# Kernel optimization log

Hardware: AMD Instinct MI355X
Metric: run time of the kernel (lower is better)

The kernel has to match this reference:

```python
import jax, jax.numpy as jnp
import numpy as np

N_NODES = 100000


def sage_conv(x, src, dst, W_l, b_l, W_r):
    # PyG SAGEConv (aggr='mean'): out = lin_l(mean_j x_j) + lin_r(x_i)
    msg = x[src]  # [E, d] gather of source-node features
    agg = jax.ops.segment_sum(msg, dst, num_segments=N_NODES)  # [N, d]
    deg = jax.ops.segment_sum(jnp.ones((src.shape[0],), x.dtype), dst,
                              num_segments=N_NODES)
    mean = agg / jnp.clip(deg, 1.0, None)[:, None]
    return mean @ W_l.T + b_l + x @ W_r.T


def setup_inputs() -> dict:
    key = jax.random.key(0)
    ks = jax.random.split(key, 12)
    d_in, d_h, d_out, n_edges = 64, 64, 2, 1200000
    s = 1.0 / np.sqrt(d_h)
    inp = {
        "x": jax.random.normal(ks[0], (N_NODES, d_in), dtype=jnp.float32),
        "edge_index": jax.random.randint(ks[1], (2, n_edges), 0, N_NODES,
                                         dtype=jnp.int64),
        "W_l1": jax.random.uniform(ks[2], (d_h, d_in), jnp.float32, -s, s),
        "b_l1": jax.random.uniform(ks[3], (d_h,), jnp.float32, -s, s),
        "W_r1": jax.random.uniform(ks[4], (d_h, d_in), jnp.float32, -s, s),
        "W_l2": jax.random.uniform(ks[5], (d_h, d_h), jnp.float32, -s, s),
        "b_l2": jax.random.uniform(ks[6], (d_h,), jnp.float32, -s, s),
        "W_r2": jax.random.uniform(ks[7], (d_h, d_h), jnp.float32, -s, s),
        "W_c": jax.random.uniform(ks[8], (d_out, d_h), jnp.float32, -s, s),
        "b_c": jax.random.uniform(ks[9], (d_out,), jnp.float32, -s, s),
    }
    return inp


def reference(x, edge_index, W_l1, b_l1, W_r1, W_l2, b_l2, W_r2, W_c, b_c):
    src, dst = edge_index[0], edge_index[1]
    # layer 1 + relu (dropout is identity in eval mode)
    h = jax.nn.relu(sage_conv(x, src, dst, W_l1, b_l1, W_r1))
    # layer 2 (no relu per forward())
    h = sage_conv(h, src, dst, W_l2, b_l2, W_r2)
    # classifier
    return h @ W_c.T + b_c
```

## Files before the change

### kernel.cpp

```cpp
#include <hip/hip_runtime.h>

#define N_NODES 100000
#define D 64
#define NTILES 3125
#define NBUCK 391
#define NBLK_A 512
#define GCNT_N (NBUCK * NBLK_A)
#define NCHUNK ((GCNT_N + 255) / 256)
#define NTILE_T (N_NODES / 32)
#define TROW 72

typedef __attribute__((ext_vector_type(8))) short short8;
typedef __attribute__((ext_vector_type(16))) float f32x16;
union Pack8 { uint4 u; short8 s; };

__device__ __forceinline__ unsigned f2bf(float f) {
  unsigned u = __float_as_uint(f);
  return (u + 0x7fffu + ((u >> 16) & 1u)) >> 16;
}
#define BF_LO(u) __uint_as_float(((unsigned)(u)) << 16)
#define BF_HI(u) __uint_as_float(((unsigned)(u)) & 0xffff0000u)


__global__ __launch_bounds__(256) void passA_count(const int* __restrict__ dst,
                                                   int* __restrict__ gcnt,
                                                   int nE, int ec) {
  __shared__ int cnt[NBUCK];
  int t = threadIdx.x, blk = blockIdx.x;
  for (int i = t; i < NBUCK; i += 256) cnt[i] = 0;
  __syncthreads();
  int e0 = blk * ec, e1 = min(e0 + ec, nE);
  for (int e = e0 + t; e < e1; e += 256) atomicAdd(&cnt[dst[e] >> 8], 1);
  __syncthreads();
  for (int b = t; b < NBUCK; b += 256) gcnt[b * NBLK_A + blk] = cnt[b];
}

__global__ void gscan_p1(const int* __restrict__ g, int* __restrict__ csum) {
  int t = threadIdx.x, b = blockIdx.x;
  int i = b * 256 + t;
  int v = (i < GCNT_N) ? g[i] : 0;
  for (int off = 32; off; off >>= 1) v += __shfl_down(v, off);
  __shared__ int ws4[4];
  if ((t & 63) == 0) ws4[t >> 6] = v;
  __syncthreads();
  if (t == 0) csum[b] = ws4[0] + ws4[1] + ws4[2] + ws4[3];
}

__global__ void gscan_p2(int* __restrict__ csum, int nB) {
  __shared__ int s[1024];
  int t = threadIdx.x;
  int orig = (t < nB) ? csum[t] : 0;
  s[t] = orig;
  __syncthreads();
  for (int off = 1; off < 1024; off <<= 1) {
    int v = (t >= off) ? s[t - off] : 0;
    __syncthreads();
    s[t] += v;
    __syncthreads();
  }
  if (t < nB) csum[t] = s[t] - orig;
}

__global__ void gscan_p3(int* __restrict__ g, const int* __restrict__ csum) {
  __shared__ int s[256];
  int t = threadIdx.x, b = blockIdx.x;
  int i = b * 256 + t;
  int d = (i < GCNT_N) ? g[i] : 0;
  s[t] = d;
  __syncthreads();
  for (int off = 1; off < 256; off <<= 1) {
    int v = (t >= off) ? s[t - off] : 0;
    __syncthreads();
    s[t] += v;
    __syncthreads();
  }
  if (i < GCNT_N) g[i] = s[t] - d + csum[b];
}

__global__ __launch_bounds__(256) void passC_place(const int* __restrict__ src,
                                                   const int* __restrict__ dst,
                                                   const int* __restrict__ S,
                                                   uint2* __restrict__ pairs,
                                                   int nE, int ec) {
  __shared__ int cur[NBUCK];
  int t = threadIdx.x, blk = blockIdx.x;
  for (int b = t; b < NBUCK; b += 256) cur[b] = S[b * NBLK_A + blk];
  __syncthreads();
  int e0 = blk * ec, e1 = min(e0 + ec, nE);
  for (int e = e0 + t; e < e1; e += 256) {
    int d = dst[e];
    int p = atomicAdd(&cur[d >> 8], 1);
    pairs[p] = make_uint2((unsigned)d, (unsigned)src[e]);
  }
}

__global__ __launch_bounds__(256) void passD_csr(const uint2* __restrict__ pairs,
                                                 const int* __restrict__ S,
                                                 int* __restrict__ rowstart,
                                                 int* __restrict__ degI,
                                                 uint2* __restrict__ srt,
                                                 int nE) {
  __shared__ int lh[256];
  __shared__ int sc[256];
  __shared__ int cur[256];
  int t = threadIdx.x, b = blockIdx.x;
  int base = S[b * NBLK_A];
  int end = (b == NBUCK - 1) ? nE : S[(b + 1) * NBLK_A];
  lh[t] = 0;
  __syncthreads();
  for (int p = base + t; p < end; p += 256) atomicAdd(&lh[pairs[p].x & 255], 1);
  __syncthreads();
  int d = lh[t];
  sc[t] = d;
  __syncthreads();
  for (int off = 1; off < 256; off <<= 1) {
    int v = (t >= off) ? sc[t - off] : 0;
    __syncthreads();
    sc[t] += v;
    __syncthreads();
  }
  int ex = sc[t] - d;
  int node = b * 256 + t;
  if (node < N_NODES) {
    rowstart[node] = base + ex;
    degI[node] = d;
  }
  cur[t] = base + ex;
  __syncthreads();
  for (int p = base + t; p < end; p += 256) {
    uint2 e = pairs[p];
    int slot = atomicAdd(&cur[e.x & 255], 1);
    srt[slot] = e;
  }
}

__global__ __launch_bounds__(256) void prep_kernel(
    const float* __restrict__ Wc, const float* __restrict__ Wl2,
    const float* __restrict__ Wr2, const float* __restrict__ bl2,
    const float* __restrict__ bc, const float* __restrict__ Wl1,
    const float* __restrict__ Wr1, float* __restrict__ A2,
    float* __restrict__ B2, float* __restrict__ bfv,
    unsigned short* __restrict__ wcat) {
  int t = threadIdx.x;
  for (int i = t; i < 8192; i += 256)
    wcat[i] = (unsigned short)f2bf((i < 4096) ? Wl1[i] : Wr1[i - 4096]);
  if (t < 128) {
    int c = t >> 6, k = t & 63;
    float sa = 0.f, sb = 0.f;
    for (int j = 0; j < 64; ++j) {
      float w = Wc[c * 64 + j];
      sa = fmaf(w, Wl2[j * 64 + k], sa);
      sb = fmaf(w, Wr2[j * 64 + k], sb);
    }
    A2[c * 64 + k] = sa;
    B2[c * 64 + k] = sb;
  }
  if (t < 2) {
    float s = bc[t];
    for (int j = 0; j < 64; ++j) s = fmaf(Wc[t * 64 + j], bl2[j], s);
    bfv[t] = s;
  }
}

__global__ __launch_bounds__(256) void transform_mfma(
    const float* __restrict__ x, const unsigned short* __restrict__ wcat,
    const float* __restrict__ bl, unsigned short* __restrict__ t1,
    unsigned short* __restrict__ r1b) {
  int tid = threadIdx.x, lane = tid & 63;
  int l31 = lane & 31, hi = lane >> 5;

  short8 af[4][4];
#pragma unroll
  for (int jt = 0; jt < 4; ++jt)
#pragma unroll
    for (int kk = 0; kk < 4; ++kk)
      af[jt][kk] = *(const short8*)(wcat + (jt * 32 + l31) * 64 + kk * 16 + 8 * hi);

  const f32x16 Z = {0.f, 0.f, 0.f, 0.f, 0.f, 0.f, 0.f, 0.f,
                    0.f, 0.f, 0.f, 0.f, 0.f, 0.f, 0.f, 0.f};
  const float4* x4 = (const float4*)x;

  int gw = (blockIdx.x * 256 + tid) >> 6;
  int nW = (gridDim.x * 256) >> 6;

  for (int tile = gw; tile < NTILE_T; tile += nW) {
    int node = tile * 32 + l31;
    f32x16 acc[4] = {Z, Z, Z, Z};
#pragma unroll
    for (int kk = 0; kk < 4; ++kk) {
      float4 fa = x4[(size_t)node * 16 + kk * 4 + 2 * hi];
      float4 fb = x4[(size_t)node * 16 + kk * 4 + 2 * hi + 1];
      Pack8 pk;
      pk.u.x = f2bf(fa.x) | (f2bf(fa.y) << 16);
      pk.u.y = f2bf(fa.z) | (f2bf(fa.w) << 16);
      pk.u.z = f2bf(fb.x) | (f2bf(fb.y) << 16);
      pk.u.w = f2bf(fb.z) | (f2bf(fb.w) << 16);
      acc[0] = __builtin_amdgcn_mfma_f32_32x32x16_bf16(af[0][kk], pk.s, acc[0], 0, 0, 0);
      acc[1] = __builtin_amdgcn_mfma_f32_32x32x16_bf16(af[1][kk], pk.s, acc[1], 0, 0, 0);
      acc[2] = __builtin_amdgcn_mfma_f32_32x32x16_bf16(af[2][kk], pk.s, acc[2], 0, 0, 0);
      acc[3] = __builtin_amdgcn_mfma_f32_32x32x16_bf16(af[3][kk], pk.s, acc[3], 0, 0, 0);
    }
#pragma unroll
    for (int jt = 0; jt < 2; ++jt)
#pragma unroll
      for (int rg = 0; rg < 4; ++rg) {
        int j0 = jt * 32 + 8 * rg + 4 * hi;
        uint2 p;
        p.x = f2bf(acc[jt][4 * rg + 0]) | (f2bf(acc[jt][4 * rg + 1]) << 16);
        p.y = f2bf(acc[jt][4 * rg + 2]) | (f2bf(acc[jt][4 * rg + 3]) << 16);
        *(uint2*)(t1 + (size_t)node * 64 + j0) = p;
      }
#pragma unroll
    for (int jt = 2; jt < 4; ++jt)
#pragma unroll
      for (int rg = 0; rg < 4; ++rg) {
        int j0 = (jt - 2) * 32 + 8 * rg + 4 * hi;
        float4 bv = ((const float4*)bl)[j0 >> 2];
        uint2 p;
        p.x = f2bf(acc[jt][4 * rg + 0] + bv.x) |
              (f2bf(acc[jt][4 * rg + 1] + bv.y) << 16);
        p.y = f2bf(acc[jt][4 * rg + 2] + bv.z) |
              (f2bf(acc[jt][4 * rg + 3] + bv.w) << 16);
        *(uint2*)(r1b + (size_t)node * 64 + j0) = p;
      }
  }
}

__global__ __launch_bounds__(256) void tile_g1(
    const uint2* __restrict__ srt, const int* __restrict__ rowstart,
    const unsigned short* __restrict__ t1,
    const unsigned short* __restrict__ r1b, const float* __restrict__ A2,
    const float* __restrict__ B2, float2* __restrict__ g2,
    float2* __restrict__ s2, int nE) {
  __shared__ float pAB[4][64];
  __shared__ unsigned short stg[4][2][16 * TROW];
  __shared__ int ideg[4][64];
  int t = threadIdx.x, lane = t & 63, w = t >> 6;
  pAB[t >> 6][t & 63] = (t < 128) ? A2[t] : B2[t - 128];
  __syncthreads();

  int tile = blockIdx.x;
  int base = rowstart[tile * 32];
  int end = (tile == NTILES - 1) ? nE : rowstart[(tile + 1) * 32];
  int l31 = lane & 31, hi = lane >> 5;
  int o = lane >> 3, j8 = lane & 7;
  unsigned short* stA = &stg[w][0][0];
  unsigned short* stB = &stg[w][1][0];

  int ngAll = (end > base) ? ((end - base + 15) >> 4) : 0;
  int gper = (ngAll + 3) >> 2;
  int wbase = base + min(w * gper, ngAll) * 16;
  int wend = min(base + min((w + 1) * gper, ngAll) * 16, end);

  const f32x16 Z = {0.f, 0.f, 0.f, 0.f, 0.f, 0.f, 0.f, 0.f,
                    0.f, 0.f, 0.f, 0.f, 0.f, 0.f, 0.f, 0.f};
  f32x16 acc0 = Z, acc1 = Z;
  int degc = 0;
  int ng = (wend > wbase) ? ((wend - wbase + 15) >> 4) : 0;

  uint2 prA = make_uint2(0u, 0u), prB = make_uint2(0u, 0u);
  int cntA = 0, cntB = 0;
  uint4 vA0 = make_uint4(0, 0, 0, 0), vA1 = vA0, vB0 = vA0, vB1 = vA0;
  if (ng > 0) {
    prA = srt[min(wbase + (lane & 15), nE - 1)];
    cntA = min(wend - wbase, 16);
    int s0 = __shfl((int)prA.y, o), s1 = __shfl((int)prA.y, 8 + o);
    vA0 = *(const uint4*)(t1 + (size_t)((o < cntA) ? s0 : 0) * 64 + j8 * 8);
    vA1 = *(const uint4*)(t1 + (size_t)((8 + o < cntA) ? s1 : 0) * 64 + j8 * 8);
  }
  if (ng > 1) {
    int nb = wbase + 16;
    prB = srt[min(nb + (lane & 15), nE - 1)];
    cntB = min(wend - nb, 16);
    int s0 = __shfl((int)prB.y, o), s1 = __shfl((int)prB.y, 8 + o);
    vB0 = *(const uint4*)(t1 + (size_t)((o < cntB) ? s0 : 0) * 64 + j8 * 8);
    vB1 = *(const uint4*)(t1 + (size_t)((8 + o < cntB) ? s1 : 0) * 64 + j8 * 8);
  }

  for (int gg = 0; gg < ng; gg += 2) {
    bool hasB = (gg + 1 < ng);
    *(uint4*)(stA + o * TROW + j8 * 8) = vA0;
    *(uint4*)(stA + (8 + o) * TROW + j8 * 8) = vA1;
    if (hasB) {
      *(uint4*)(stB + o * TROW + j8 * 8) = vB0;
      *(uint4*)(stB + (8 + o) * TROW + j8 * 8) = vB1;
    }
    unsigned amA[8], amB[8];
#pragma unroll
    for (int m = 0; m < 8; ++m) {
      int e = 8 * hi + m;
      int dv = __shfl((int)prA.x, e);
      bool ok = (e < cntA) && ((dv & 31) == l31);
      amA[m] = ok ? 0x3F80u : 0u;
      degc += (amA[m] >> 7) & 1;
    }
    if (hasB) {
#pragma unroll
      for (int m = 0; m < 8; ++m) {
        int e = 8 * hi + m;
        int dv = __shfl((int)prB.x, e);
        bool ok = (e < cntB) && ((dv & 31) == l31);
        amB[m] = ok ? 0x3F80u : 0u;
        degc += (amB[m] >> 7) & 1;
      }
    }
    if (gg + 2 < ng) {
      int nb = wbase + (gg + 2) * 16;
      prA = srt[min(nb + (lane & 15), nE - 1)];
      cntA = min(wend - nb, 16);
      int s0 = __shfl((int)prA.y, o), s1 = __shfl((int)prA.y, 8 + o);
      vA0 = *(const uint4*)(t1 + (size_t)((o < cntA) ? s0 : 0) * 64 + j8 * 8);
      vA1 = *(const uint4*)(t1 + (size_t)((8 + o < cntA) ? s1 : 0) * 64 + j8 * 8);
    }
    if (gg + 3 < ng) {
      int nb = wbase + (gg + 3) * 16;
      prB = srt[min(nb + (lane & 15), nE - 1)];
      cntB = min(wend - nb, 16);
      int s0 = __shfl((int)prB.y, o), s1 = __shfl((int)prB.y, 8 + o);
      vB0 = *(const uint4*)(t1 + (size_t)((o < cntB) ? s0 : 0) * 64 + j8 * 8);
      vB1 = *(const uint4*)(t1 + (size_t)((8 + o < cntB) ? s1 : 0) * 64 + j8 * 8);
    }
    {
      Pack8 I;
      I.u.x = amA[0] | (amA[1] << 16);
      I.u.y = amA[2] | (amA[3] << 16);
      I.u.z = amA[4] | (amA[5] << 16);
      I.u.w = amA[6] | (amA[7] << 16);
      unsigned short b0[8], b1[8];
#pragma unroll
      for (int m = 0; m < 8; ++m) {
        b0[m] = stA[(8 * hi + m) * TROW + l31];
        b1[m] = stA[(8 * hi + m) * TROW + 32 + l31];
      }
      Pack8 F0, F1;
      F0.u.x = b0[0] | ((unsigned)b0[1] << 16);
      F0.u.y = b0[2] | ((unsigned)b0[3] << 16);
      F0.u.z = b0[4] | ((unsigned)b0[5] << 16);
      F0.u.w = b0[6] | ((unsigned)b0[7] << 16);
      F1.u.x = b1[0] | ((unsigned)b1[1] << 16);
      F1.u.y = b1[2] | ((unsigned)b1[3] << 16);
      F1.u.z = b1[4] | ((unsigned)b1[5] << 16);
      F1.u.w = b1[6] | ((unsigned)b1[7] << 16);
      acc0 = __builtin_amdgcn_mfma_f32_32x32x16_bf16(F0.s, I.s, acc0, 0, 0, 0);
      acc1 = __builtin_amdgcn_mfma_f32_32x32x16_bf16(F1.s, I.s, acc1, 0, 0, 0);
    }
    if (hasB) {
      Pack8 I;
      I.u.x = amB[0] | (amB[1] << 16);
      I.u.y = amB[2] | (amB[3] << 16);
      I.u.z = amB[4] | (amB[5] << 16);
      I.u.w = amB[6] | (amB[7] << 16);
      unsigned short b0[8], b1[8];
#pragma unroll
      for (int m = 0; m < 8; ++m) {
        b0[m] = stB[(8 * hi + m) * TROW + l31];
        b1[m] = stB[(8 * hi + m) * TROW + 32 + l31];
      }
      Pack8 F0, F1;
      F0.u.x = b0[0] | ((unsigned)b0[1] << 16);
      F0.u.y = b0[2] | ((unsigned)b0[3] << 16);
      F0.u.z = b0[4] | ((unsigned)b0[5] << 16);
      F0.u.w = b0[6] | ((unsigned)b0[7] << 16);
      F1.u.x = b1[0] | ((unsigned)b1[1] << 16);
      F1.u.y = b1[2] | ((unsigned)b1[3] << 16);
      F1.u.z = b1[4] | ((unsigned)b1[5] << 16);
      F1.u.w = b1[6] | ((unsigned)b1[7] << 16);
      acc0 = __builtin_amdgcn_mfma_f32_32x32x16_bf16(F0.s, I.s, acc0, 0, 0, 0);
      acc1 = __builtin_amdgcn_mfma_f32_32x32x16_bf16(F1.s, I.s, acc1, 0, 0, 0);
    }
  }

  ideg[w][lane] = degc;
  __syncthreads();
  float* red = (float*)&stg[0][0][0];
  for (int r = 1; r < 4; ++r) {
    if (w == r) {
#pragma unroll
      for (int i = 0; i < 16; ++i) {
        red[i * 64 + lane] = acc0[i];
        red[(16 + i) * 64 + lane] = acc1[i];
      }
    }
    __syncthreads();
    if (w == 0) {
#pragma unroll
      for (int i = 0; i < 16; ++i) {
        acc0[i] += red[i * 64 + lane];
        acc1[i] += red[(16 + i) * 64 + lane];
      }
    }
    __syncthreads();
  }

  if (w == 0) {
    int dtot = ideg[0][lane] + ideg[1][lane] + ideg[2][lane] + ideg[3][lane];
    float degf = (float)(dtot + __shfl_xor(dtot, 32));
    float inv = 1.f / fmaxf(degf, 1.f);
    int node = tile * 32 + l31;
    float d0 = 0.f, d1 = 0.f, d2 = 0.f, d3 = 0.f;
#pragma unroll
    for (int fb = 0; fb < 2; ++fb) {
#pragma unroll
      for (int q4 = 0; q4 < 4; ++q4) {
        int f0 = fb * 32 + q4 * 8 + 4 * hi;
        uint2 rv = *(const uint2*)(r1b + (size_t)node * 64 + f0);
        float bias[4] = {BF_LO(rv.x), BF_HI(rv.x), BF_LO(rv.y), BF_HI(rv.y)};
#pragma unroll
        for (int j = 0; j < 4; ++j) {
          float a = fb ? acc1[q4 * 4 + j] : acc0[q4 * 4 + j];
          float hv = fmaxf(fmaf(a, inv, bias[j]), 0.f);
          int f = f0 + j;
          d0 = fmaf(hv, pAB[0][f], d0);
          d1 = fmaf(hv, pAB[1][f], d1);
          d2 = fmaf(hv, pAB[2][f], d2);
          d3 = fmaf(hv, pAB[3][f], d3);
        }
      }
    }
    d0 += __shfl_xor(d0, 32);
    d1 += __shfl_xor(d1, 32);
    d2 += __shfl_xor(d2, 32);
    d3 += __shfl_xor(d3, 32);
    if (hi == 0) {
      g2[node] = make_float2(d0, d1);
      s2[node] = make_float2(d2, d3);
    }
  }
}

__global__ __launch_bounds__(256) void gather2_kernel(
    const int* __restrict__ rowstart, const int* __restrict__ degI,
    const uint2* __restrict__ srt, const float2* __restrict__ g2,
    const float2* __restrict__ s2, const float* __restrict__ bfv,
    float* __restrict__ out, int nE) {
  int tid = threadIdx.x, lane = tid & 63;
  int q = lane >> 4, l16 = lane & 15;
  float bf0 = bfv[0], bf1 = bfv[1];
  int gq = ((blockIdx.x * 256 + tid) >> 6) * 4 + q;
  int strideN = ((gridDim.x * 256) >> 6) * 4;
  for (int n = gq; n < N_NODES; n += strideN) {
    int rs = rowstart[n], dg = degI[n];
    float s0 = 0.f, s1 = 0.f;
    for (int base = 0; base < dg; base += 16) {
      int e = base + l16;
      int a = (int)srt[min(rs + ((e < dg) ? e : 0), nE - 1)].y;
      float2 v = g2[a];
      float m = (e < dg) ? 1.f : 0.f;
      s0 = fmaf(v.x, m, s0);
      s1 = fmaf(v.y, m, s1);
    }
    s0 += __shfl_xor(s0, 1); s0 += __shfl_xor(s0, 2);
    s0 += __shfl_xor(s0, 4); s0 += __shfl_xor(s0, 8);
    s1 += __shfl_xor(s1, 1); s1 += __shfl_xor(s1, 2);
    s1 += __shfl_xor(s1, 4); s1 += __shfl_xor(s1, 8);
    if (l16 == 0) {
      float inv = 1.f / (float)max(dg, 1);
      float2 sv = s2[n];
      out[(size_t)n * 2 + 0] = fmaf(s0, inv, sv.x) + bf0;
      out[(size_t)n * 2 + 1] = fmaf(s1, inv, sv.y) + bf1;
    }
  }
}

extern "C" void kernel_launch(void* const* d_in, const int* in_sizes, int n_in,
                              void* d_out, int out_size, void* d_ws,
                              size_t ws_size, hipStream_t stream) {
  const float* x   = (const float*)d_in[0];
  const int*   ei  = (const int*)d_in[1];
  const float* Wl1 = (const float*)d_in[2];
  const float* bl1 = (const float*)d_in[3];
  const float* Wr1 = (const float*)d_in[4];
  const float* Wl2 = (const float*)d_in[5];
  const float* bl2 = (const float*)d_in[6];
  const float* Wr2 = (const float*)d_in[7];
  const float* Wc  = (const float*)d_in[8];
  const float* bc  = (const float*)d_in[9];
  float* out = (float*)d_out;

  int nE = in_sizes[1] / 2;
  const int* src = ei;
  const int* dst = ei + nE;

  unsigned short* t1 = (unsigned short*)d_ws;
  uint2* pairs = (uint2*)d_ws;
  uint2* srt = (uint2*)(t1 + (size_t)N_NODES * D);
  unsigned short* r1b = (unsigned short*)(srt + nE);
  float2* g2 = (float2*)(r1b + (size_t)N_NODES * D);
  float2* s2 = g2 + N_NODES;
  float* A2 = (float*)(s2 + N_NODES);
  float* B2 = A2 + 128;
  float* bfv = B2 + 128;
  unsigned short* wcat = (unsigned short*)(bfv + 4);
  int* degI = (int*)(wcat + 8192);
  int* rowstart = degI + N_NODES;
  int* gcnt = rowstart + N_NODES;
  int* csum = gcnt + GCNT_N;

  int ec = (nE + NBLK_A - 1) / NBLK_A;

  passA_count<<<NBLK_A, 256, 0, stream>>>(dst, gcnt, nE, ec);
  gscan_p1<<<NCHUNK, 256, 0, stream>>>(gcnt, csum);
  gscan_p2<<<1, 1024, 0, stream>>>(csum, NCHUNK);
  gscan_p3<<<NCHUNK, 256, 0, stream>>>(gcnt, csum);
  passC_place<<<NBLK_A, 256, 0, stream>>>(src, dst, gcnt, pairs, nE, ec);
  passD_csr<<<NBUCK, 256, 0, stream>>>(pairs, gcnt, rowstart, degI, srt, nE);

  prep_kernel<<<1, 256, 0, stream>>>(Wc, Wl2, Wr2, bl2, bc, Wl1, Wr1, A2, B2,
                                     bfv, wcat);
  transform_mfma<<<512, 256, 0, stream>>>(x, wcat, bl1, t1, r1b);

  tile_g1<<<NTILES, 256, 0, stream>>>(srt, rowstart, t1, r1b, A2, B2, g2, s2,
                                      nE);
  gather2_kernel<<<512, 256, 0, stream>>>(rowstart, degI, srt, g2, s2, bfv,
                                          out, nE);
}
```

Measured before the change: 143.5 us.

## Merge CSR placement with weight prep and CSR build with MFMA transform

Folds the single-block weight prep kernel into the edge placement kernel as an extra block. It also runs the per-bucket CSR sort and the bf16 MFMA feature transform as disjoint block ranges of one launch, so the two independent stages can overlap. The workspace is rearranged so that pairs no longer alias t1, which makes the concurrent write safe. The count/place block count is halved, which changes per-block edge chunk sizes and scan size. This cuts two launches and lets the transform fill idle CUs, at the cost of more workspace and a mixed-resource kernel.

```diff
diff --git a/kernel.cpp b/kernel.cpp
--- a/kernel.cpp
+++ b/kernel.cpp
@@ -4,11 +4,12 @@
 #define D 64
 #define NTILES 3125
 #define NBUCK 391
-#define NBLK_A 512
+#define NBLK_A 256
 #define GCNT_N (NBUCK * NBLK_A)
 #define NCHUNK ((GCNT_N + 255) / 256)
 #define NTILE_T (N_NODES / 32)
 #define TROW 72
+#define TBLK 512
 
 typedef __attribute__((ext_vector_type(8))) short short8;
 typedef __attribute__((ext_vector_type(16))) float f32x16;
@@ -77,152 +78,149 @@
   if (i < GCNT_N) g[i] = s[t] - d + csum[b];
 }
 
-__global__ __launch_bounds__(256) void passC_place(const int* __restrict__ src,
-                                                   const int* __restrict__ dst,
-                                                   const int* __restrict__ S,
-                                                   uint2* __restrict__ pairs,
-                                                   int nE, int ec) {
-  __shared__ int cur[NBUCK];
-  int t = threadIdx.x, blk = blockIdx.x;
-  for (int b = t; b < NBUCK; b += 256) cur[b] = S[b * NBLK_A + blk];
-  __syncthreads();
-  int e0 = blk * ec, e1 = min(e0 + ec, nE);
-  for (int e = e0 + t; e < e1; e += 256) {
-    int d = dst[e];
-    int p = atomicAdd(&cur[d >> 8], 1);
-    pairs[p] = make_uint2((unsigned)d, (unsigned)src[e]);
-  }
-}
-
-__global__ __launch_bounds__(256) void passD_csr(const uint2* __restrict__ pairs,
-                                                 const int* __restrict__ S,
-                                                 int* __restrict__ rowstart,
-                                                 int* __restrict__ degI,
-                                                 uint2* __restrict__ srt,
-                                                 int nE) {
-  __shared__ int lh[256];
-  __shared__ int sc[256];
-  __shared__ int cur[256];
-  int t = threadIdx.x, b = blockIdx.x;
-  int base = S[b * NBLK_A];
-  int end = (b == NBUCK - 1) ? nE : S[(b + 1) * NBLK_A];
-  lh[t] = 0;
-  __syncthreads();
-  for (int p = base + t; p < end; p += 256) atomicAdd(&lh[pairs[p].x & 255], 1);
-  __syncthreads();
-  int d = lh[t];
-  sc[t] = d;
-  __syncthreads();
-  for (int off = 1; off < 256; off <<= 1) {
-    int v = (t >= off) ? sc[t - off] : 0;
-    __syncthreads();
-    sc[t] += v;
-    __syncthreads();
-  }
-  int ex = sc[t] - d;
-  int node = b * 256 + t;
-  if (node < N_NODES) {
-    rowstart[node] = base + ex;
-    degI[node] = d;
-  }
-  cur[t] = base + ex;
-  __syncthreads();
-  for (int p = base + t; p < end; p += 256) {
-    uint2 e = pairs[p];
-    int slot = atomicAdd(&cur[e.x & 255], 1);
-    srt[slot] = e;
-  }
-}
-
-__global__ __launch_bounds__(256) void prep_kernel(
+__global__ __launch_bounds__(256) void passC_prep(
+    const int* __restrict__ src, const int* __restrict__ dst,
+    const int* __restrict__ S, uint2* __restrict__ pairs, int nE, int ec,
     const float* __restrict__ Wc, const float* __restrict__ Wl2,
     const float* __restrict__ Wr2, const float* __restrict__ bl2,
     const float* __restrict__ bc, const float* __restrict__ Wl1,
     const float* __restrict__ Wr1, float* __restrict__ A2,
     float* __restrict__ B2, float* __restrict__ bfv,
     unsigned short* __restrict__ wcat) {
-  int t = threadIdx.x;
-  for (int i = t; i < 8192; i += 256)
-    wcat[i] = (unsigned short)f2bf((i < 4096) ? Wl1[i] : Wr1[i - 4096]);
-  if (t < 128) {
-    int c = t >> 6, k = t & 63;
-    float sa = 0.f, sb = 0.f;
-    for (int j = 0; j < 64; ++j) {
-      float w = Wc[c * 64 + j];
-      sa = fmaf(w, Wl2[j * 64 + k], sa);
-      sb = fmaf(w, Wr2[j * 64 + k], sb);
-    }
-    A2[c * 64 + k] = sa;
-    B2[c * 64 + k] = sb;
-  }
-  if (t < 2) {
-    float s = bc[t];
-    for (int j = 0; j < 64; ++j) s = fmaf(Wc[t * 64 + j], bl2[j], s);
-    bfv[t] = s;
-  }
-}
-
-__global__ __launch_bounds__(256) void transform_mfma(
+  __shared__ int cur[NBUCK];
+  int t = threadIdx.x, blk = blockIdx.x;
+  if (blk < NBLK_A) {
+    for (int b = t; b < NBUCK; b += 256) cur[b] = S[b * NBLK_A + blk];
+    __syncthreads();
+    int e0 = blk * ec, e1 = min(e0 + ec, nE);
+    for (int e = e0 + t; e < e1; e += 256) {
+      int d = dst[e];
+      int p = atomicAdd(&cur[d >> 8], 1);
+      pairs[p] = make_uint2((unsigned)d, (unsigned)src[e]);
+    }
+  } else {
+    for (int i = t; i < 8192; i += 256)
+      wcat[i] = (unsigned short)f2bf((i < 4096) ? Wl1[i] : Wr1[i - 4096]);
+    if (t < 128) {
+      int c = t >> 6, k = t & 63;
+      float sa = 0.f, sb = 0.f;
+      for (int j = 0; j < 64; ++j) {
+        float w = Wc[c * 64 + j];
+        sa = fmaf(w, Wl2[j * 64 + k], sa);
+        sb = fmaf(w, Wr2[j * 64 + k], sb);
+      }
+      A2[c * 64 + k] = sa;
+      B2[c * 64 + k] = sb;
+    }
+    if (t < 2) {
+      float s = bc[t];
+      for (int j = 0; j < 64; ++j) s = fmaf(Wc[t * 64 + j], bl2[j], s);
+      bfv[t] = s;
+    }
+  }
+}
+
+__global__ __launch_bounds__(256) void passD_transform(
+    const uint2* __restrict__ pairs, const int* __restrict__ S,
+    int* __restrict__ rowstart, int* __restrict__ degI,
+    uint2* __restrict__ srt, int nE,
     const float* __restrict__ x, const unsigned short* __restrict__ wcat,
     const float* __restrict__ bl, unsigned short* __restrict__ t1,
     unsigned short* __restrict__ r1b) {
-  int tid = threadIdx.x, lane = tid & 63;
-  int l31 = lane & 31, hi = lane >> 5;
-
-  short8 af[4][4];
-#pragma unroll
-  for (int jt = 0; jt < 4; ++jt)
-#pragma unroll
-    for (int kk = 0; kk < 4; ++kk)
-      af[jt][kk] = *(const short8*)(wcat + (jt * 32 + l31) * 64 + kk * 16 + 8 * hi);
-
-  const f32x16 Z = {0.f, 0.f, 0.f, 0.f, 0.f, 0.f, 0.f, 0.f,
-                    0.f, 0.f, 0.f, 0.f, 0.f, 0.f, 0.f, 0.f};
-  const float4* x4 = (const float4*)x;
-
-  int gw = (blockIdx.x * 256 + tid) >> 6;
-  int nW = (gridDim.x * 256) >> 6;
-
-  for (int tile = gw; tile < NTILE_T; tile += nW) {
-    int node = tile * 32 + l31;
-    f32x16 acc[4] = {Z, Z, Z, Z};
-#pragma unroll
-    for (int kk = 0; kk < 4; ++kk) {
-      float4 fa = x4[(size_t)node * 16 + kk * 4 + 2 * hi];
-      float4 fb = x4[(size_t)node * 16 + kk * 4 + 2 * hi + 1];
-      Pack8 pk;
-      pk.u.x = f2bf(fa.x) | (f2bf(fa.y) << 16);
-      pk.u.y = f2bf(fa.z) | (f2bf(fa.w) << 16);
-      pk.u.z = f2bf(fb.x) | (f2bf(fb.y) << 16);
-      pk.u.w = f2bf(fb.z) | (f2bf(fb.w) << 16);
-      acc[0] = __builtin_amdgcn_mfma_f32_32x32x16_bf16(af[0][kk], pk.s, acc[0], 0, 0, 0);
-      acc[1] = __builtin_amdgcn_mfma_f32_32x32x16_bf16(af[1][kk], pk.s, acc[1], 0, 0, 0);
-      acc[2] = __builtin_amdgcn_mfma_f32_32x32x16_bf16(af[2][kk], pk.s, acc[2], 0, 0, 0);
-      acc[3] = __builtin_amdgcn_mfma_f32_32x32x16_bf16(af[3][kk], pk.s, acc[3], 0, 0, 0);
-    }
-#pragma unroll
-    for (int jt = 0; jt < 2; ++jt)
-#pragma unroll
-      for (int rg = 0; rg < 4; ++rg) {
-        int j0 = jt * 32 + 8 * rg + 4 * hi;
-        uint2 p;
-        p.x = f2bf(acc[jt][4 * rg + 0]) | (f2bf(acc[jt][4 * rg + 1]) << 16);
-        p.y = f2bf(acc[jt][4 * rg + 2]) | (f2bf(acc[jt][4 * rg + 3]) << 16);
-        *(uint2*)(t1 + (size_t)node * 64 + j0) = p;
-      }
-#pragma unroll
-    for (int jt = 2; jt < 4; ++jt)
-#pragma unroll
-      for (int rg = 0; rg < 4; ++rg) {
-        int j0 = (jt - 2) * 32 + 8 * rg + 4 * hi;
-        float4 bv = ((const float4*)bl)[j0 >> 2];
-        uint2 p;
-        p.x = f2bf(acc[jt][4 * rg + 0] + bv.x) |
-              (f2bf(acc[jt][4 * rg + 1] + bv.y) << 16);
-        p.y = f2bf(acc[jt][4 * rg + 2] + bv.z) |
-              (f2bf(acc[jt][4 * rg + 3] + bv.w) << 16);
-        *(uint2*)(r1b + (size_t)node * 64 + j0) = p;
-      }
+  __shared__ int lh[256];
+  __shared__ int sc[256];
+  __shared__ int cur[256];
+  int t = threadIdx.x;
+  if (blockIdx.x < NBUCK) {
+    int b = blockIdx.x;
+    int base = S[b * NBLK_A];
+    int end = (b == NBUCK - 1) ? nE : S[(b + 1) * NBLK_A];
+    lh[t] = 0;
+    __syncthreads();
+    for (int p = base + t; p < end; p += 256) atomicAdd(&lh[pairs[p].x & 255], 1);
+    __syncthreads();
+    int d = lh[t];
+    sc[t] = d;
+    __syncthreads();
+    for (int off = 1; off < 256; off <<= 1) {
+      int v = (t >= off) ? sc[t - off] : 0;
+      __syncthreads();
+      sc[t] += v;
+      __syncthreads();
+    }
+    int ex = sc[t] - d;
+    int node = b * 256 + t;
+    if (node < N_NODES) {
+      rowstart[node] = base + ex;
+      degI[node] = d;
+    }
+    cur[t] = base + ex;
+    __syncthreads();
+    for (int p = base + t; p < end; p += 256) {
+      uint2 e = pairs[p];
+      int slot = atomicAdd(&cur[e.x & 255], 1);
+      srt[slot] = e;
+    }
+  } else {
+    int lane = t & 63;
+    int l31 = lane & 31, hi = lane >> 5;
+
+    short8 af[4][4];
+#pragma unroll
+    for (int jt = 0; jt < 4; ++jt)
+#pragma unroll
+      for (int kk = 0; kk < 4; ++kk)
+        af[jt][kk] =
+            *(const short8*)(wcat + (jt * 32 + l31) * 64 + kk * 16 + 8 * hi);
+
+    const f32x16 Z = {0.f, 0.f, 0.f, 0.f, 0.f, 0.f, 0.f, 0.f,
+                      0.f, 0.f, 0.f, 0.f, 0.f, 0.f, 0.f, 0.f};
+    const float4* x4 = (const float4*)x;
+
+    int gw = ((blockIdx.x - NBUCK) * 256 + t) >> 6;
+    int nW = (TBLK * 256) >> 6;
+
+    for (int tile = gw; tile < NTILE_T; tile += nW) {
+      int node = tile * 32 + l31;
+      f32x16 acc[4] = {Z, Z, Z, Z};
+#pragma unroll
+      for (int kk = 0; kk < 4; ++kk) {
+        float4 fa = x4[(size_t)node * 16 + kk * 4 + 2 * hi];
+        float4 fb = x4[(size_t)node * 16 + kk * 4 + 2 * hi + 1];
+        Pack8 pk;
+        pk.u.x = f2bf(fa.x) | (f2bf(fa.y) << 16);
+        pk.u.y = f2bf(fa.z) | (f2bf(fa.w) << 16);
+        pk.u.z = f2bf(fb.x) | (f2bf(fb.y) << 16);
+        pk.u.w = f2bf(fb.z) | (f2bf(fb.w) << 16);
+        acc[0] = __builtin_amdgcn_mfma_f32_32x32x16_bf16(af[0][kk], pk.s, acc[0], 0, 0, 0);
+        acc[1] = __builtin_amdgcn_mfma_f32_32x32x16_bf16(af[1][kk], pk.s, acc[1], 0, 0, 0);
+        acc[2] = __builtin_amdgcn_mfma_f32_32x32x16_bf16(af[2][kk], pk.s, acc[2], 0, 0, 0);
+        acc[3] = __builtin_amdgcn_mfma_f32_32x32x16_bf16(af[3][kk], pk.s, acc[3], 0, 0, 0);
+      }
+#pragma unroll
+      for (int jt = 0; jt < 2; ++jt)
+#pragma unroll
+        for (int rg = 0; rg < 4; ++rg) {
+          int j0 = jt * 32 + 8 * rg + 4 * hi;
+          uint2 p;
+          p.x = f2bf(acc[jt][4 * rg + 0]) | (f2bf(acc[jt][4 * rg + 1]) << 16);
+          p.y = f2bf(acc[jt][4 * rg + 2]) | (f2bf(acc[jt][4 * rg + 3]) << 16);
+          *(uint2*)(t1 + (size_t)node * 64 + j0) = p;
+        }
+#pragma unroll
+      for (int jt = 2; jt < 4; ++jt)
+#pragma unroll
+        for (int rg = 0; rg < 4; ++rg) {
+          int j0 = (jt - 2) * 32 + 8 * rg + 4 * hi;
+          float4 bv = ((const float4*)bl)[j0 >> 2];
+          uint2 p;
+          p.x = f2bf(acc[jt][4 * rg + 0] + bv.x) |
+                (f2bf(acc[jt][4 * rg + 1] + bv.y) << 16);
+          p.y = f2bf(acc[jt][4 * rg + 2] + bv.z) |
+                (f2bf(acc[jt][4 * rg + 3] + bv.w) << 16);
+          *(uint2*)(r1b + (size_t)node * 64 + j0) = p;
+        }
+    }
   }
 }
 
@@ -481,10 +479,10 @@
   const int* src = ei;
   const int* dst = ei + nE;
 
-  unsigned short* t1 = (unsigned short*)d_ws;
   uint2* pairs = (uint2*)d_ws;
-  uint2* srt = (uint2*)(t1 + (size_t)N_NODES * D);
-  unsigned short* r1b = (unsigned short*)(srt + nE);
+  uint2* srt = pairs + nE;
+  unsigned short* t1 = (unsigned short*)(srt + nE);
+  unsigned short* r1b = t1 + (size_t)N_NODES * D;
   float2* g2 = (float2*)(r1b + (size_t)N_NODES * D);
   float2* s2 = g2 + N_NODES;
   float* A2 = (float*)(s2 + N_NODES);
@@ -502,13 +500,12 @@
   gscan_p1<<<NCHUNK, 256, 0, stream>>>(gcnt, csum);
   gscan_p2<<<1, 1024, 0, stream>>>(csum, NCHUNK);
   gscan_p3<<<NCHUNK, 256, 0, stream>>>(gcnt, csum);
-  passC_place<<<NBLK_A, 256, 0, stream>>>(src, dst, gcnt, pairs, nE, ec);
-  passD_csr<<<NBUCK, 256, 0, stream>>>(pairs, gcnt, rowstart, degI, srt, nE);
-
-  prep_kernel<<<1, 256, 0, stream>>>(Wc, Wl2, Wr2, bl2, bc, Wl1, Wr1, A2, B2,
-                                     bfv, wcat);
-  transform_mfma<<<512, 256, 0, stream>>>(x, wcat, bl1, t1, r1b);
-
+  passC_prep<<<NBLK_A + 1, 256, 0, stream>>>(src, dst, gcnt, pairs, nE, ec,
+                                             Wc, Wl2, Wr2, bl2, bc, Wl1, Wr1,
+                                             A2, B2, bfv, wcat);
+  passD_transform<<<NBUCK + TBLK, 256, 0, stream>>>(pairs, gcnt, rowstart,
+                                                    degI, srt, nE, x, wcat,
+                                                    bl1, t1, r1b);
   tile_g1<<<NTILES, 256, 0, stream>>>(srt, rowstart, t1, r1b, A2, B2, g2, s2,
                                       nE);
   gather2_kernel<<<512, 256, 0, stream>>>(rowstart, degI, srt, g2, s2, bfv,
```

Result: faster. 131.1 us (-8.6%).
